# Kernel optimization log

Hardware: AMD Instinct MI355X
Metric: run time of the kernel (lower is better)

## Reference

```python
import jax, jax.numpy as jnp
import numpy as np

N = 50000
E = 1600000
IN_C, HID_C, OUT_C, EDGE_D = 128, 64, 64, 32
NEG_SLOPE = 0.2


def _add_self_loops(edge_index, edge_attr, n):
    # PyG add_self_loops with fill_value='mean': loop attr = mean of incoming edge attrs per node
    src, dst = edge_index[0], edge_index[1]
    attr_sum = jax.ops.segment_sum(edge_attr, dst, num_segments=n)          # [N, D]
    cnt = jax.ops.segment_sum(jnp.ones((edge_attr.shape[0],), edge_attr.dtype), dst, num_segments=n)
    loop_attr = attr_sum / jnp.maximum(cnt, 1.0)[:, None]                   # [N, D]
    loop = jnp.arange(n, dtype=src.dtype)
    src = jnp.concatenate([src, loop])
    dst = jnp.concatenate([dst, loop])
    edge_attr = jnp.concatenate([edge_attr, loop_attr], axis=0)
    return src, dst, edge_attr


def gat_conv(x, edge_index, edge_attr, W, We, att_src, att_dst, att_edge, bias, n):
    # heads=1, concat=True (PyG defaults); att_* have shape [1, C]
    src, dst, ea = _add_self_loops(edge_index, edge_attr, n)
    h = x @ W                                   # [N, C]
    a_src = jnp.sum(h * att_src, axis=-1)       # [N]
    a_dst = jnp.sum(h * att_dst, axis=-1)       # [N]
    he = ea @ We                                # [E+N, C]
    a_edge = jnp.sum(he * att_edge, axis=-1)    # [E+N]
    alpha = a_src[src] + a_dst[dst] + a_edge
    alpha = jax.nn.leaky_relu(alpha, NEG_SLOPE)
    # segment softmax over destination nodes (every node has a self-loop)
    m = jax.ops.segment_max(alpha, dst, num_segments=n)
    alpha = jnp.exp(alpha - m[dst])
    denom = jax.ops.segment_sum(alpha, dst, num_segments=n)
    alpha = alpha / (denom[dst] + 1e-16)
    out = jax.ops.segment_sum(alpha[:, None] * h[src], dst, num_segments=n)  # [N, C]
    return out + bias


def setup_inputs() -> dict:
    key = jax.random.key(0)
    ks = jax.random.split(key, 12)
    def g(k, shape, scale=1.0):
        return jax.random.normal(k, shape, dtype=jnp.float32) * scale
    x = g(ks[0], (N, IN_C))
    edge_index = jax.random.randint(ks[1], (2, E), 0, N, dtype=jnp.int64)
    edge_attr = g(ks[2], (E, EDGE_D))
    s1 = 1.0 / np.sqrt(IN_C)
    s2 = 1.0 / np.sqrt(HID_C)
    se = 1.0 / np.sqrt(EDGE_D)
    return {
        "x": x, "edge_index": edge_index, "edge_attr": edge_attr,
        "W1": g(ks[3], (IN_C, HID_C), s1), "We1": g(ks[4], (EDGE_D, HID_C), se),
        "att_src1": g(ks[5], (1, HID_C), s2), "att_dst1": g(ks[6], (1, HID_C), s2),
        "att_edge1": g(ks[7], (1, HID_C), s2), "b1": jnp.zeros((HID_C,), jnp.float32),
        "W2": g(ks[8], (HID_C, OUT_C), s2), "We2": g(ks[9], (EDGE_D, OUT_C), se),
        "att_src2": g(ks[10], (1, OUT_C), s2), "att_dst2": g(ks[11], (1, OUT_C), s2),
        "att_edge2": g(jax.random.fold_in(key, 99), (1, OUT_C), s2),
        "b2": jnp.zeros((OUT_C,), jnp.float32),
    }


def reference(x, edge_index, edge_attr,
              W1, We1, att_src1, att_dst1, att_edge1, b1,
              W2, We2, att_src2, att_dst2, att_edge2, b2):
    h = gat_conv(x, edge_index, edge_attr, W1, We1, att_src1, att_dst1, att_edge1, b1, N)
    h = jax.nn.relu(h)
    # F.dropout(p=0.1, training=self.training): identity in eval mode
    out = gat_conv(h, edge_index, edge_attr, W2, We2, att_src2, att_dst2, att_edge2, b2, N)
    return out
```

## Files before the change

kernel.cpp:

```cpp
#include <hip/hip_runtime.h>
#include <hip/hip_bf16.h>

__device__ __forceinline__ unsigned f2bf_rne(float f) {
    unsigned u = __float_as_uint(f);
    u += 0x7FFFu + ((u >> 16) & 1u);
    return u >> 16;
}
__device__ __forceinline__ float bf_lo(unsigned p) { return __uint_as_float(p << 16); }
__device__ __forceinline__ float bf_hi(unsigned p) { return __uint_as_float(p & 0xFFFF0000u); }
template <int I> __device__ __forceinline__ float bfsel(unsigned p) {
    return (I == 0) ? bf_lo(p) : bf_hi(p);
}

__global__ __launch_bounds__(256)
void init_kernel(int* __restrict__ cnt, int n,
                 const float* __restrict__ We1, const float* __restrict__ ae1v,
                 const float* __restrict__ We2, const float* __restrict__ ae2v,
                 float* __restrict__ we1, float* __restrict__ we2) {
    int i = blockIdx.x * 256 + threadIdx.x;
    if (i < n) cnt[i] = 0;
    if (blockIdx.x == 0 && threadIdx.x >= 64 && threadIdx.x < 128) {
        int t = threadIdx.x - 64;
        const float* W = (t < 32) ? We1 : We2;
        const float* a = (t < 32) ? ae1v : ae2v;
        float* o       = (t < 32) ? we1 : we2;
        int k = t & 31;
        float s = 0.f;
        for (int c = 0; c < 64; ++c) s += W[k * 64 + c] * a[c];
        o[k] = s;
    }
}

__global__ __launch_bounds__(256)
void edge_pass_kernel(const float4* __restrict__ ea, const int* __restrict__ eidx,
                      const float* __restrict__ we1g, const float* __restrict__ we2g,
                      int* __restrict__ cnt, uint2* __restrict__ pack8,
                      unsigned* __restrict__ meta, int E) {
    int tid = threadIdx.x;
    int q = tid & 7;
    int e = blockIdx.x * 32 + (tid >> 3);
    if (e >= E) return;
    float4 w1 = ((const float4*)we1g)[q];
    float4 w2 = ((const float4*)we2g)[q];
    float4 v = ea[(size_t)e * 8 + q];
    float a1 = v.x * w1.x + v.y * w1.y + v.z * w1.z + v.w * w1.w;
    float a2 = v.x * w2.x + v.y * w2.y + v.z * w2.z + v.w * w2.w;
#pragma unroll
    for (int off = 1; off < 8; off <<= 1) {
        a1 += __shfl_xor(a1, off, 64);
        a2 += __shfl_xor(a2, off, 64);
    }
    if (q == 0) {
        int src = eidx[e];
        int dst = eidx[E + e];
        int rk = atomicAdd(&cnt[dst], 1);
        pack8[e] = make_uint2((unsigned)src, f2bf_rne(a1) | (f2bf_rne(a2) << 16));
        meta[e] = ((unsigned)rk << 16) | (unsigned)dst;
    }
}

__global__ __launch_bounds__(256)
void scanA_kernel(const int* __restrict__ cnt, int* __restrict__ bsum, int n) {
    int idx = blockIdx.x * 256 + threadIdx.x;
    int v = (idx < n) ? cnt[idx] : 0;
#pragma unroll
    for (int off = 32; off >= 1; off >>= 1) v += __shfl_xor(v, off, 64);
    __shared__ int ws[4];
    int lane = threadIdx.x & 63, wid = threadIdx.x >> 6;
    if (lane == 0) ws[wid] = v;
    __syncthreads();
    if (threadIdx.x == 0) bsum[blockIdx.x] = ws[0] + ws[1] + ws[2] + ws[3];
}

__global__ void scanB_kernel(const int* __restrict__ bsum, int* __restrict__ boff, int nb) {
    int lane = threadIdx.x;
    int carry = 0;
    for (int base = 0; base < nb; base += 64) {
        int idx = base + lane;
        int v = (idx < nb) ? bsum[idx] : 0;
        int s = v;
#pragma unroll
        for (int off = 1; off < 64; off <<= 1) {
            int t = __shfl_up(s, off, 64);
            if (lane >= off) s += t;
        }
        if (idx < nb) boff[idx] = carry + s - v;
        carry += __shfl(s, 63, 64);
    }
}

__global__ __launch_bounds__(256)
void scanC_kernel(const int* __restrict__ cnt, const int* __restrict__ boff,
                  int* __restrict__ row_ptr, int n, int E) {
    __shared__ int ws[4];
    __shared__ int woff[4];
    int idx = blockIdx.x * 256 + threadIdx.x;
    int lane = threadIdx.x & 63, wid = threadIdx.x >> 6;
    int v = (idx < n) ? cnt[idx] : 0;
    int s = v;
#pragma unroll
    for (int off = 1; off < 64; off <<= 1) {
        int t = __shfl_up(s, off, 64);
        if (lane >= off) s += t;
    }
    if (lane == 63) ws[wid] = s;
    __syncthreads();
    if (threadIdx.x == 0) {
        int run = 0;
        for (int w = 0; w < 4; ++w) { int t = ws[w]; woff[w] = run; run += t; }
    }
    __syncthreads();
    if (idx < n) row_ptr[idx] = boff[blockIdx.x] + woff[wid] + s - v;
    if (idx == 0) row_ptr[n] = E;
}

__global__ __launch_bounds__(256)
void scatter_kernel(const uint2* __restrict__ pack8, const unsigned* __restrict__ meta,
                    const int* __restrict__ row_ptr, uint2* __restrict__ s_rec, int E) {
    int e = blockIdx.x * 256 + threadIdx.x;
    if (e >= E) return;
    unsigned m = meta[e];
    int dst = (int)(m & 0xFFFFu);
    int rk  = (int)(m >> 16);
    s_rec[row_ptr[dst] + rk] = pack8[e];
}

template <int INC>
__global__ __launch_bounds__(256)
void gemm_kernel(const float* __restrict__ X, const float* __restrict__ W,
                 const float* __restrict__ asv, const float* __restrict__ adv,
                 __hip_bfloat16* __restrict__ H, float* __restrict__ a_src,
                 float* __restrict__ a_dst, int n) {
    constexpr int LDW = INC + 4;
    __shared__ float Wl[64 * LDW];
    for (int t = threadIdx.x; t < INC * 64; t += 256) {
        int k = t >> 6, c = t & 63;
        Wl[c * LDW + k] = W[t];
    }
    __syncthreads();
    int wid = threadIdx.x >> 6, lane = threadIdx.x & 63;
    int i = blockIdx.x * 4 + wid;
    if (i >= n) return;
    const float4* xr = (const float4*)(X + (size_t)i * INC);
    const float4* wr = (const float4*)(Wl + lane * LDW);
    float acc = 0.f;
#pragma unroll
    for (int k4 = 0; k4 < INC / 4; ++k4) {
        float4 xv = xr[k4];
        float4 wv = wr[k4];
        acc += xv.x * wv.x + xv.y * wv.y + xv.z * wv.z + xv.w * wv.w;
    }
    H[(size_t)i * 64 + lane] = __float2bfloat16(acc);
    float s = acc * asv[lane];
    float d = acc * adv[lane];
#pragma unroll
    for (int off = 32; off >= 1; off >>= 1) {
        s += __shfl_xor(s, off, 64);
        d += __shfl_xor(d, off, 64);
    }
    if (lane == 0) { a_src[i] = s; a_dst[i] = d; }
}

__device__ __forceinline__ float4 bf4_to_f4(ushort4 u) {
    float4 f;
    f.x = __uint_as_float((unsigned)u.x << 16);
    f.y = __uint_as_float((unsigned)u.y << 16);
    f.z = __uint_as_float((unsigned)u.z << 16);
    f.w = __uint_as_float((unsigned)u.w << 16);
    return f;
}

template <int AEIDX, bool RELU>
__global__ __launch_bounds__(256)
void agg_fused_kernel(const int* __restrict__ row_ptr, const uint2* __restrict__ s_rec,
                      const float* __restrict__ a_srcv, const float* __restrict__ a_dstv,
                      const ushort4* __restrict__ H4, const float* __restrict__ bias,
                      float* __restrict__ out, int n) {
    __shared__ uint2 wl[4][128];
    int wid = threadIdx.x >> 6, lane = threadIdx.x & 63;
    int i = blockIdx.x * 4 + wid;
    if (i >= n) return;
    int start = row_ptr[i], end = row_ptr[i + 1];
    int deg = end - start;
    float adst = a_dstv[i];

    float w0 = 0.f, w1 = 0.f;
    int src0 = 0, src1 = 0;
    float aeloc = 0.f, dloc = 0.f;
    {
        int j = start + lane;
        if (j < end) {
            uint2 r = s_rec[j];
            float ae = bfsel<AEIDX>(r.y);
            src0 = (int)r.x;
            float a = a_srcv[src0] + adst + ae;
            a = a > 0.f ? a : 0.2f * a;
            w0 = __expf(a);
            aeloc += ae; dloc += w0;
        }
    }
    if (deg > 64) {
        int j = start + 64 + lane;
        if (j < end) {
            uint2 r = s_rec[j];
            float ae = bfsel<AEIDX>(r.y);
            src1 = (int)r.x;
            float a = a_srcv[src1] + adst + ae;
            a = a > 0.f ? a : 0.2f * a;
            w1 = __expf(a);
            aeloc += ae; dloc += w1;
        }
    }
    for (int base = start + 128; base < end; base += 64) {
        int j = base + lane;
        if (j < end) {
            uint2 r = s_rec[j];
            float ae = bfsel<AEIDX>(r.y);
            int s = (int)r.x;
            float a = a_srcv[s] + adst + ae;
            a = a > 0.f ? a : 0.2f * a;
            aeloc += ae; dloc += __expf(a);
        }
    }
#pragma unroll
    for (int off = 32; off >= 1; off >>= 1) {
        aeloc += __shfl_xor(aeloc, off, 64);
        dloc  += __shfl_xor(dloc, off, 64);
    }
    float ael = aeloc / (float)(deg > 0 ? deg : 1);
    float als = a_srcv[i] + adst + ael;
    als = als > 0.f ? als : 0.2f * als;
    float wself = __expf(als);
    float inv = 1.f / (dloc + wself + 1e-16f);

    wl[wid][lane]      = make_uint2((unsigned)src0, __float_as_uint(w0));
    wl[wid][64 + lane] = make_uint2((unsigned)src1, __float_as_uint(w1));

    int sub = lane >> 4;
    int c4  = lane & 15;
    float4 acc = make_float4(0.f, 0.f, 0.f, 0.f);
    int mainCnt = deg < 128 ? deg : 128;
#pragma unroll 4
    for (int r = 0; r < mainCnt; r += 4) {
        uint2 sw = wl[wid][r + sub];
        float w = __uint_as_float(sw.y);
        float4 hv = bf4_to_f4(H4[(size_t)((sw.x << 4) | (unsigned)c4)]);
        acc.x += w * hv.x; acc.y += w * hv.y;
        acc.z += w * hv.z; acc.w += w * hv.w;
    }
    for (int j = start + 128; j < end; j += 4) {
        int jj = j + sub;
        if (jj < end) {
            uint2 r = s_rec[jj];
            float ae = bfsel<AEIDX>(r.y);
            int s = (int)r.x;
            float a = a_srcv[s] + adst + ae;
            a = a > 0.f ? a : 0.2f * a;
            float w = __expf(a);
            float4 hv = bf4_to_f4(H4[(size_t)(((unsigned)s << 4) | (unsigned)c4)]);
            acc.x += w * hv.x; acc.y += w * hv.y;
            acc.z += w * hv.z; acc.w += w * hv.w;
        }
    }
#pragma unroll
    for (int off = 16; off <= 32; off <<= 1) {
        acc.x += __shfl_xor(acc.x, off, 64);
        acc.y += __shfl_xor(acc.y, off, 64);
        acc.z += __shfl_xor(acc.z, off, 64);
        acc.w += __shfl_xor(acc.w, off, 64);
    }
    float4 hv = bf4_to_f4(H4[(size_t)(((unsigned)i << 4) | (unsigned)c4)]);
    float4 bv = ((const float4*)bias)[c4];
    float4 o;
    o.x = (acc.x + wself * hv.x) * inv + bv.x;
    o.y = (acc.y + wself * hv.y) * inv + bv.y;
    o.z = (acc.z + wself * hv.z) * inv + bv.z;
    o.w = (acc.w + wself * hv.w) * inv + bv.w;
    if (RELU) {
        o.x = fmaxf(o.x, 0.f); o.y = fmaxf(o.y, 0.f);
        o.z = fmaxf(o.z, 0.f); o.w = fmaxf(o.w, 0.f);
    }
    if (sub == 0) ((float4*)out)[(size_t)i * 16 + c4] = o;
}

extern "C" void kernel_launch(void* const* d_in, const int* in_sizes, int n_in,
                              void* d_out, int out_size, void* d_ws, size_t ws_size,
                              hipStream_t stream) {
    const float* x        = (const float*)d_in[0];
    const int*   eidx     = (const int*)d_in[1];
    const float* eattr    = (const float*)d_in[2];
    const float* W1       = (const float*)d_in[3];
    const float* We1      = (const float*)d_in[4];
    const float* att_src1 = (const float*)d_in[5];
    const float* att_dst1 = (const float*)d_in[6];
    const float* att_edge1= (const float*)d_in[7];
    const float* b1       = (const float*)d_in[8];
    const float* W2       = (const float*)d_in[9];
    const float* We2      = (const float*)d_in[10];
    const float* att_src2 = (const float*)d_in[11];
    const float* att_dst2 = (const float*)d_in[12];
    const float* att_edge2= (const float*)d_in[13];
    const float* b2       = (const float*)d_in[14];
    float* out = (float*)d_out;

    const int n = in_sizes[0] / 128;
    const int E = in_sizes[1] / 2;

    char* ws = (char*)d_ws;
    size_t off = 0;
    auto carve = [&](size_t bytes) {
        char* p = ws + off;
        off = (off + bytes + 255) & ~(size_t)255;
        return p;
    };
    const int nblkScan = (n + 255) / 256;
    float*    we1    = (float*)carve(32 * 4);
    float*    we2    = (float*)carve(32 * 4);
    int*      cnt    = (int*)carve((size_t)n * 4);
    int*      bsum   = (int*)carve((size_t)nblkScan * 4);
    int*      boff   = (int*)carve((size_t)nblkScan * 4);
    int*      row_ptr= (int*)carve((size_t)(n + 1) * 4);
    uint2*    pack8  = (uint2*)carve((size_t)E * 8);
    unsigned* meta   = (unsigned*)carve((size_t)E * 4);
    uint2*    s_rec  = (uint2*)carve((size_t)E * 8);
    __hip_bfloat16* bufA = (__hip_bfloat16*)carve((size_t)n * 64 * 2);
    float*    bufB   = (float*)carve((size_t)n * 64 * 4);
    float*    a_src  = (float*)carve((size_t)n * 4);
    float*    a_dst  = (float*)carve((size_t)n * 4);

    init_kernel<<<nblkScan, 256, 0, stream>>>(cnt, n, We1, att_edge1,
                                              We2, att_edge2, we1, we2);

    edge_pass_kernel<<<(E + 31) / 32, 256, 0, stream>>>((const float4*)eattr, eidx,
                                                        we1, we2, cnt, pack8, meta, E);
    scanA_kernel<<<nblkScan, 256, 0, stream>>>(cnt, bsum, n);
    scanB_kernel<<<1, 64, 0, stream>>>(bsum, boff, nblkScan);
    scanC_kernel<<<nblkScan, 256, 0, stream>>>(cnt, boff, row_ptr, n, E);

    scatter_kernel<<<(E + 255) / 256, 256, 0, stream>>>(pack8, meta, row_ptr, s_rec, E);

    int ngrid = (n + 3) / 4;
    gemm_kernel<128><<<ngrid, 256, 0, stream>>>(x, W1, att_src1, att_dst1,
                                                bufA, a_src, a_dst, n);
    agg_fused_kernel<0, true><<<ngrid, 256, 0, stream>>>(row_ptr, s_rec, a_src,
                                                         a_dst, (const ushort4*)bufA,
                                                         b1, bufB, n);
    gemm_kernel<64><<<ngrid, 256, 0, stream>>>(bufB, W2, att_src2, att_dst2,
                                               bufA, a_src, a_dst, n);
    agg_fused_kernel<1, false><<<ngrid, 256, 0, stream>>>(row_ptr, s_rec, a_src,
                                                          a_dst, (const ushort4*)bufA,
                                                          b2, out, n);
}
```

Before: 297.2 us.

## Split aggregation into weight pass and two column-half gather passes

The fused aggregation kernel is split in two. A first kernel computes per-edge softmax weights into a global src/weight array and stores the per-node self-loop weight and inverse denominator. Two gather kernels then each handle half of the feature columns (8 lanes per row, 8 edges in flight), so each pass touches a smaller slice of H for better cache locality. In exchange it adds extra launches, writes and reads an E-sized weight array, and reads row_ptr and the edge list twice per layer.

```diff
diff --git a/kernel.cpp b/kernel.cpp
--- a/kernel.cpp
+++ b/kernel.cpp
@@ -170,13 +170,11 @@
     return f;
 }
 
-template <int AEIDX, bool RELU>
-__global__ __launch_bounds__(256)
-void agg_fused_kernel(const int* __restrict__ row_ptr, const uint2* __restrict__ s_rec,
-                      const float* __restrict__ a_srcv, const float* __restrict__ a_dstv,
-                      const ushort4* __restrict__ H4, const float* __restrict__ bias,
-                      float* __restrict__ out, int n) {
-    __shared__ uint2 wl[4][128];
+template <int AEIDX>
+__global__ __launch_bounds__(256)
+void aggA_kernel(const int* __restrict__ row_ptr, const uint2* __restrict__ s_rec,
+                 const float* __restrict__ a_srcv, const float* __restrict__ a_dstv,
+                 uint2* __restrict__ srcw, float2* __restrict__ winv, int n) {
     int wid = threadIdx.x >> 6, lane = threadIdx.x & 63;
     int i = blockIdx.x * 4 + wid;
     if (i >= n) return;
@@ -187,29 +185,25 @@
     float w0 = 0.f, w1 = 0.f;
     int src0 = 0, src1 = 0;
     float aeloc = 0.f, dloc = 0.f;
-    {
-        int j = start + lane;
-        if (j < end) {
-            uint2 r = s_rec[j];
-            float ae = bfsel<AEIDX>(r.y);
-            src0 = (int)r.x;
-            float a = a_srcv[src0] + adst + ae;
-            a = a > 0.f ? a : 0.2f * a;
-            w0 = __expf(a);
-            aeloc += ae; dloc += w0;
-        }
-    }
-    if (deg > 64) {
-        int j = start + 64 + lane;
-        if (j < end) {
-            uint2 r = s_rec[j];
-            float ae = bfsel<AEIDX>(r.y);
-            src1 = (int)r.x;
-            float a = a_srcv[src1] + adst + ae;
-            a = a > 0.f ? a : 0.2f * a;
-            w1 = __expf(a);
-            aeloc += ae; dloc += w1;
-        }
+    int j0 = start + lane;
+    if (j0 < end) {
+        uint2 r = s_rec[j0];
+        float ae = bfsel<AEIDX>(r.y);
+        src0 = (int)r.x;
+        float a = a_srcv[src0] + adst + ae;
+        a = a > 0.f ? a : 0.2f * a;
+        w0 = __expf(a);
+        aeloc += ae; dloc += w0;
+    }
+    int j1 = start + 64 + lane;
+    if (deg > 64 && j1 < end) {
+        uint2 r = s_rec[j1];
+        float ae = bfsel<AEIDX>(r.y);
+        src1 = (int)r.x;
+        float a = a_srcv[src1] + adst + ae;
+        a = a > 0.f ? a : 0.2f * a;
+        w1 = __expf(a);
+        aeloc += ae; dloc += w1;
     }
     for (int base = start + 128; base < end; base += 64) {
         int j = base + lane;
@@ -219,7 +213,9 @@
             int s = (int)r.x;
             float a = a_srcv[s] + adst + ae;
             a = a > 0.f ? a : 0.2f * a;
-            aeloc += ae; dloc += __expf(a);
+            float w = __expf(a);
+            aeloc += ae; dloc += w;
+            srcw[j] = make_uint2((unsigned)s, __float_as_uint(w));
         }
     }
 #pragma unroll
@@ -233,54 +229,70 @@
     float wself = __expf(als);
     float inv = 1.f / (dloc + wself + 1e-16f);
 
-    wl[wid][lane]      = make_uint2((unsigned)src0, __float_as_uint(w0));
-    wl[wid][64 + lane] = make_uint2((unsigned)src1, __float_as_uint(w1));
-
-    int sub = lane >> 4;
-    int c4  = lane & 15;
+    if (j0 < end) srcw[j0] = make_uint2((unsigned)src0, __float_as_uint(w0));
+    if (deg > 64 && j1 < end) srcw[j1] = make_uint2((unsigned)src1, __float_as_uint(w1));
+    if (lane == 0) winv[i] = make_float2(wself, inv);
+}
+
+template <int HALF, bool RELU>
+__global__ __launch_bounds__(256)
+void aggB_kernel(const int* __restrict__ row_ptr, const uint2* __restrict__ srcw,
+                 const float2* __restrict__ winv, const ushort4* __restrict__ H4,
+                 const float* __restrict__ bias, float* __restrict__ out, int n) {
+    __shared__ uint2 wl[4][128];
+    int wid = threadIdx.x >> 6, lane = threadIdx.x & 63;
+    int i = blockIdx.x * 4 + wid;
+    if (i >= n) return;
+    int start = row_ptr[i], end = row_ptr[i + 1];
+    int deg = end - start;
+    {
+        int j = start + lane;
+        wl[wid][lane] = (j < end) ? srcw[j] : make_uint2(0u, 0u);
+        int j2 = start + 64 + lane;
+        wl[wid][64 + lane] = (j2 < end) ? srcw[j2] : make_uint2(0u, 0u);
+    }
+    int sub = lane >> 3;
+    int c8  = lane & 7;
     float4 acc = make_float4(0.f, 0.f, 0.f, 0.f);
     int mainCnt = deg < 128 ? deg : 128;
 #pragma unroll 4
-    for (int r = 0; r < mainCnt; r += 4) {
+    for (int r = 0; r < mainCnt; r += 8) {
         uint2 sw = wl[wid][r + sub];
         float w = __uint_as_float(sw.y);
-        float4 hv = bf4_to_f4(H4[(size_t)((sw.x << 4) | (unsigned)c4)]);
+        float4 hv = bf4_to_f4(H4[(size_t)((sw.x << 4) | (unsigned)(HALF * 8 + c8))]);
         acc.x += w * hv.x; acc.y += w * hv.y;
         acc.z += w * hv.z; acc.w += w * hv.w;
     }
-    for (int j = start + 128; j < end; j += 4) {
+    for (int j = start + 128; j < end; j += 8) {
         int jj = j + sub;
         if (jj < end) {
-            uint2 r = s_rec[jj];
-            float ae = bfsel<AEIDX>(r.y);
-            int s = (int)r.x;
-            float a = a_srcv[s] + adst + ae;
-            a = a > 0.f ? a : 0.2f * a;
-            float w = __expf(a);
-            float4 hv = bf4_to_f4(H4[(size_t)(((unsigned)s << 4) | (unsigned)c4)]);
+            uint2 sw = srcw[jj];
+            float w = __uint_as_float(sw.y);
+            float4 hv = bf4_to_f4(H4[(size_t)((sw.x << 4) | (unsigned)(HALF * 8 + c8))]);
             acc.x += w * hv.x; acc.y += w * hv.y;
             acc.z += w * hv.z; acc.w += w * hv.w;
         }
     }
 #pragma unroll
-    for (int off = 16; off <= 32; off <<= 1) {
+    for (int off = 8; off <= 32; off <<= 1) {
         acc.x += __shfl_xor(acc.x, off, 64);
         acc.y += __shfl_xor(acc.y, off, 64);
         acc.z += __shfl_xor(acc.z, off, 64);
         acc.w += __shfl_xor(acc.w, off, 64);
     }
-    float4 hv = bf4_to_f4(H4[(size_t)(((unsigned)i << 4) | (unsigned)c4)]);
-    float4 bv = ((const float4*)bias)[c4];
+    float2 wi = winv[i];
+    float4 hv = bf4_to_f4(H4[(size_t)(((unsigned)i << 4) | (unsigned)(HALF * 8 + c8))]);
+    float4 bv = ((const float4*)bias)[HALF * 8 + c8];
     float4 o;
-    o.x = (acc.x + wself * hv.x) * inv + bv.x;
-    o.y = (acc.y + wself * hv.y) * inv + bv.y;
-    o.z = (acc.z + wself * hv.z) * inv + bv.z;
-    o.w = (acc.w + wself * hv.w) * inv + bv.w;
+    o.x = (acc.x + wi.x * hv.x) * wi.y + bv.x;
+    o.y = (acc.y + wi.x * hv.y) * wi.y + bv.y;
+    o.z = (acc.z + wi.x * hv.z) * wi.y + bv.z;
+    o.w = (acc.w + wi.x * hv.w) * wi.y + bv.w;
     if (RELU) {
         o.x = fmaxf(o.x, 0.f); o.y = fmaxf(o.y, 0.f);
         o.z = fmaxf(o.z, 0.f); o.w = fmaxf(o.w, 0.f);
     }
-    if (sub == 0) ((float4*)out)[(size_t)i * 16 + c4] = o;
+    if (sub == 0) ((float4*)out)[(size_t)i * 16 + HALF * 8 + c8] = o;
 }
 
 extern "C" void kernel_launch(void* const* d_in, const int* in_sizes, int n_in,
@@ -323,6 +335,8 @@
     uint2*    pack8  = (uint2*)carve((size_t)E * 8);
     unsigned* meta   = (unsigned*)carve((size_t)E * 4);
     uint2*    s_rec  = (uint2*)carve((size_t)E * 8);
+    uint2*    srcw   = (uint2*)carve((size_t)E * 8);
+    float2*   winv   = (float2*)carve((size_t)n * 8);
     __hip_bfloat16* bufA = (__hip_bfloat16*)carve((size_t)n * 64 * 2);
     float*    bufB   = (float*)carve((size_t)n * 64 * 4);
     float*    a_src  = (float*)carve((size_t)n * 4);
@@ -342,12 +356,18 @@
     int ngrid = (n + 3) / 4;
     gemm_kernel<128><<<ngrid, 256, 0, stream>>>(x, W1, att_src1, att_dst1,
                                                 bufA, a_src, a_dst, n);
-    agg_fused_kernel<0, true><<<ngrid, 256, 0, stream>>>(row_ptr, s_rec, a_src,
-                                                         a_dst, (const ushort4*)bufA,
-                                                         b1, bufB, n);
+    aggA_kernel<0><<<ngrid, 256, 0, stream>>>(row_ptr, s_rec, a_src, a_dst,
+                                              srcw, winv, n);
+    aggB_kernel<0, true><<<ngrid, 256, 0, stream>>>(row_ptr, srcw, winv,
+                                                    (const ushort4*)bufA, b1, bufB, n);
+    aggB_kernel<1, true><<<ngrid, 256, 0, stream>>>(row_ptr, srcw, winv,
+                                                    (const ushort4*)bufA, b1, bufB, n);
     gemm_kernel<64><<<ngrid, 256, 0, stream>>>(bufB, W2, att_src2, att_dst2,
                                                bufA, a_src, a_dst, n);
-    agg_fused_kernel<1, false><<<ngrid, 256, 0, stream>>>(row_ptr, s_rec, a_src,
-                                                          a_dst, (const ushort4*)bufA,
-                                                          b2, out, n);
-}
+    aggA_kernel<1><<<ngrid, 256, 0, stream>>>(row_ptr, s_rec, a_src, a_dst,
+                                              srcw, winv, n);
+    aggB_kernel<0, false><<<ngrid, 256, 0, stream>>>(row_ptr, srcw, winv,
+                                                     (const ushort4*)bufA, b2, out, n);
+    aggB_kernel<1, false><<<ngrid, 256, 0, stream>>>(row_ptr, srcw, winv,
+                                                     (const ushort4*)bufA, b2, out, n);
+}
```

New measurement: 357.0 us. 1.2x slower.

## Fuse layer-2 GEMM into layer-1 aggregation and drop scanB kernel

Applied to the files above, without the earlier changes.

Layer-1 aggregation now multiplies its ReLU output row by W2 in-wave (via an LDS row staging buffer) and writes the bf16 layer-2 features and attention scalars directly. This removes the separate layer-2 GEMM launch and the fp32 intermediate buffer write and read. The scan drops its single-block middle pass: each scanC block redundantly sums all preceding block totals itself. The cost is extra per-wave ALU and W2 reads inside the aggregation kernel, plus a quadratic-ish redundant reduction over about 196 block sums.

```diff
diff --git a/kernel.cpp b/kernel.cpp
--- a/kernel.cpp
+++ b/kernel.cpp
@@ -72,30 +72,21 @@
     if (threadIdx.x == 0) bsum[blockIdx.x] = ws[0] + ws[1] + ws[2] + ws[3];
 }
 
-__global__ void scanB_kernel(const int* __restrict__ bsum, int* __restrict__ boff, int nb) {
-    int lane = threadIdx.x;
-    int carry = 0;
-    for (int base = 0; base < nb; base += 64) {
-        int idx = base + lane;
-        int v = (idx < nb) ? bsum[idx] : 0;
-        int s = v;
-#pragma unroll
-        for (int off = 1; off < 64; off <<= 1) {
-            int t = __shfl_up(s, off, 64);
-            if (lane >= off) s += t;
-        }
-        if (idx < nb) boff[idx] = carry + s - v;
-        carry += __shfl(s, 63, 64);
-    }
-}
-
-__global__ __launch_bounds__(256)
-void scanC_kernel(const int* __restrict__ cnt, const int* __restrict__ boff,
+__global__ __launch_bounds__(256)
+void scanC_kernel(const int* __restrict__ cnt, const int* __restrict__ bsum,
                   int* __restrict__ row_ptr, int n, int E) {
     __shared__ int ws[4];
     __shared__ int woff[4];
+    __shared__ int bws[4];
+    int lane = threadIdx.x & 63, wid = threadIdx.x >> 6;
+    int partial = 0;
+    for (int j = threadIdx.x; j < blockIdx.x; j += 256) partial += bsum[j];
+#pragma unroll
+    for (int off = 32; off >= 1; off >>= 1) partial += __shfl_xor(partial, off, 64);
+    if (lane == 0) bws[wid] = partial;
+    __syncthreads();
+    int boff = bws[0] + bws[1] + bws[2] + bws[3];
     int idx = blockIdx.x * 256 + threadIdx.x;
-    int lane = threadIdx.x & 63, wid = threadIdx.x >> 6;
     int v = (idx < n) ? cnt[idx] : 0;
     int s = v;
 #pragma unroll
@@ -110,7 +101,7 @@
         for (int w = 0; w < 4; ++w) { int t = ws[w]; woff[w] = run; run += t; }
     }
     __syncthreads();
-    if (idx < n) row_ptr[idx] = boff[blockIdx.x] + woff[wid] + s - v;
+    if (idx < n) row_ptr[idx] = boff + woff[wid] + s - v;
     if (idx == 0) row_ptr[n] = E;
 }
 
@@ -170,13 +161,17 @@
     return f;
 }
 
-template <int AEIDX, bool RELU>
+template <int AEIDX, bool RELU, bool FUSE_GEMM2>
 __global__ __launch_bounds__(256)
 void agg_fused_kernel(const int* __restrict__ row_ptr, const uint2* __restrict__ s_rec,
                       const float* __restrict__ a_srcv, const float* __restrict__ a_dstv,
                       const ushort4* __restrict__ H4, const float* __restrict__ bias,
-                      float* __restrict__ out, int n) {
+                      float* __restrict__ out,
+                      const float* __restrict__ W2, const float* __restrict__ as2v,
+                      const float* __restrict__ ad2v, __hip_bfloat16* __restrict__ H2,
+                      float* __restrict__ a_src2, float* __restrict__ a_dst2, int n) {
     __shared__ uint2 wl[4][128];
+    __shared__ float4 rowl[4][16];
     int wid = threadIdx.x >> 6, lane = threadIdx.x & 63;
     int i = blockIdx.x * 4 + wid;
     if (i >= n) return;
@@ -280,7 +275,31 @@
         o.x = fmaxf(o.x, 0.f); o.y = fmaxf(o.y, 0.f);
         o.z = fmaxf(o.z, 0.f); o.w = fmaxf(o.w, 0.f);
     }
-    if (sub == 0) ((float4*)out)[(size_t)i * 16 + c4] = o;
+
+    if (!FUSE_GEMM2) {
+        if (sub == 0) ((float4*)out)[(size_t)i * 16 + c4] = o;
+        return;
+    }
+
+    if (sub == 0) rowl[wid][c4] = o;
+    float acc2 = 0.f;
+#pragma unroll
+    for (int q = 0; q < 16; ++q) {
+        float4 rq = rowl[wid][q];
+        acc2 += rq.x * W2[(q * 4 + 0) * 64 + lane];
+        acc2 += rq.y * W2[(q * 4 + 1) * 64 + lane];
+        acc2 += rq.z * W2[(q * 4 + 2) * 64 + lane];
+        acc2 += rq.w * W2[(q * 4 + 3) * 64 + lane];
+    }
+    H2[(size_t)i * 64 + lane] = __float2bfloat16(acc2);
+    float s2 = acc2 * as2v[lane];
+    float d2 = acc2 * ad2v[lane];
+#pragma unroll
+    for (int off = 32; off >= 1; off >>= 1) {
+        s2 += __shfl_xor(s2, off, 64);
+        d2 += __shfl_xor(d2, off, 64);
+    }
+    if (lane == 0) { a_src2[i] = s2; a_dst2[i] = d2; }
 }
 
 extern "C" void kernel_launch(void* const* d_in, const int* in_sizes, int n_in,
@@ -318,15 +337,16 @@
     float*    we2    = (float*)carve(32 * 4);
     int*      cnt    = (int*)carve((size_t)n * 4);
     int*      bsum   = (int*)carve((size_t)nblkScan * 4);
-    int*      boff   = (int*)carve((size_t)nblkScan * 4);
     int*      row_ptr= (int*)carve((size_t)(n + 1) * 4);
     uint2*    pack8  = (uint2*)carve((size_t)E * 8);
     unsigned* meta   = (unsigned*)carve((size_t)E * 4);
     uint2*    s_rec  = (uint2*)carve((size_t)E * 8);
     __hip_bfloat16* bufA = (__hip_bfloat16*)carve((size_t)n * 64 * 2);
-    float*    bufB   = (float*)carve((size_t)n * 64 * 4);
+    __hip_bfloat16* bufB = (__hip_bfloat16*)carve((size_t)n * 64 * 2);
     float*    a_src  = (float*)carve((size_t)n * 4);
     float*    a_dst  = (float*)carve((size_t)n * 4);
+    float*    a_src2 = (float*)carve((size_t)n * 4);
+    float*    a_dst2 = (float*)carve((size_t)n * 4);
 
     init_kernel<<<nblkScan, 256, 0, stream>>>(cnt, n, We1, att_edge1,
                                               We2, att_edge2, we1, we2);
@@ -334,20 +354,17 @@
     edge_pass_kernel<<<(E + 31) / 32, 256, 0, stream>>>((const float4*)eattr, eidx,
                                                         we1, we2, cnt, pack8, meta, E);
     scanA_kernel<<<nblkScan, 256, 0, stream>>>(cnt, bsum, n);
-    scanB_kernel<<<1, 64, 0, stream>>>(bsum, boff, nblkScan);
-    scanC_kernel<<<nblkScan, 256, 0, stream>>>(cnt, boff, row_ptr, n, E);
+    scanC_kernel<<<nblkScan, 256, 0, stream>>>(cnt, bsum, row_ptr, n, E);
 
     scatter_kernel<<<(E + 255) / 256, 256, 0, stream>>>(pack8, meta, row_ptr, s_rec, E);
 
     int ngrid = (n + 3) / 4;
     gemm_kernel<128><<<ngrid, 256, 0, stream>>>(x, W1, att_src1, att_dst1,
                                                 bufA, a_src, a_dst, n);
-    agg_fused_kernel<0, true><<<ngrid, 256, 0, stream>>>(row_ptr, s_rec, a_src,
-                                                         a_dst, (const ushort4*)bufA,
-                                                         b1, bufB, n);
-    gemm_kernel<64><<<ngrid, 256, 0, stream>>>(bufB, W2, att_src2, att_dst2,
-                                               bufA, a_src, a_dst, n);
-    agg_fused_kernel<1, false><<<ngrid, 256, 0, stream>>>(row_ptr, s_rec, a_src,
-                                                          a_dst, (const ushort4*)bufA,
-                                                          b2, out, n);
-}
+    agg_fused_kernel<0, true, true><<<ngrid, 256, 0, stream>>>(
+        row_ptr, s_rec, a_src, a_dst, (const ushort4*)bufA, b1,
+        nullptr, W2, att_src2, att_dst2, bufB, a_src2, a_dst2, n);
+    agg_fused_kernel<1, false, false><<<ngrid, 256, 0, stream>>>(
+        row_ptr, s_rec, a_src2, a_dst2, (const ushort4*)bufB, b2,
+        out, nullptr, nullptr, nullptr, nullptr, nullptr, nullptr, n);
+}
```

Result: faster. 272.7 us, median of 3 (-8.3%).
